# Kernel optimization log

Measured on AMD Instinct MI355X. Metric: run time of the kernel, lower is better.

Reference implementation:

```python
import jax, jax.numpy as jnp
import numpy as np
import math

B, L, HID, H, DH = 4, 1024, 1024, 16, 64
EPS = 1e-5


def setup_inputs() -> dict:
    key = jax.random.key(0)
    ks = jax.random.split(key, 12)
    s = 0.02
    return {
        "hidden_states_query": jax.random.normal(ks[0], (B, L, HID), jnp.float32),
        "hidden_states_value": jax.random.normal(ks[1], (B, L, HID), jnp.float32),
        "attention_mask": jnp.zeros((B, 1, 1, L), jnp.float32),
        "structure_matrix": jax.random.normal(ks[2], (L, L, DH), jnp.float32) * s,
        "Wq": jax.random.normal(ks[3], (H * DH, HID), jnp.float32) * s,
        "bq": jnp.zeros((H * DH,), jnp.float32),
        "Wk": jax.random.normal(ks[4], (H * DH, HID), jnp.float32) * s,
        "bk": jnp.zeros((H * DH,), jnp.float32),
        "Wv": jax.random.normal(ks[5], (H * DH, HID), jnp.float32) * s,
        "bv": jnp.zeros((H * DH,), jnp.float32),
        "Wd": jax.random.normal(ks[6], (HID, H * DH), jnp.float32) * s,
        "bd": jnp.zeros((HID,), jnp.float32),
        "ln_gamma": jnp.ones((HID,), jnp.float32),
        "ln_beta": jnp.zeros((HID,), jnp.float32),
    }


def _heads(x):
    # [B, L, H*DH] -> [B, H, L, DH]
    b, l, _ = x.shape
    return x.reshape(b, l, H, DH).transpose(0, 2, 1, 3)


def reference(hidden_states_query, hidden_states_value, attention_mask, structure_matrix,
              Wq, bq, Wk, bk, Wv, bv, Wd, bd, ln_gamma, ln_beta):
    q = _heads(hidden_states_query @ Wq.T + bq)   # [B,H,Lq,DH]
    k = _heads(hidden_states_value @ Wk.T + bk)   # [B,H,Lk,DH]
    v = _heads(hidden_states_value @ Wv.T + bv)   # [B,H,Lk,DH]

    scores = jnp.einsum('bhld,bhrd->bhlr', q, k)
    # relative-position (structure) bias terms
    scores = scores + jnp.einsum('bhld,lrd->bhlr', q, structure_matrix)
    scores = scores + jnp.einsum('bhrd,lrd->bhlr', k, structure_matrix)
    scores = scores / math.sqrt(DH)
    scores = scores + attention_mask  # broadcast [B,1,1,Lk]

    probs = jax.nn.softmax(scores, axis=-1)
    ctx = jnp.einsum('bhlr,bhrd->bhld', probs, v)
    ctx = ctx.transpose(0, 2, 1, 3).reshape(q.shape[0], q.shape[2], H * DH)

    out = ctx @ Wd.T + bd
    x = out + hidden_states_query
    mu = jnp.mean(x, axis=-1, keepdims=True)
    var = jnp.mean(jnp.square(x - mu), axis=-1, keepdims=True)
    out = (x - mu) * jax.lax.rsqrt(var + EPS) * ln_gamma + ln_beta
    return (out, scores)
```

## Files before the change

kernel.cpp:

```cpp
#include <hip/hip_runtime.h>

typedef unsigned short u16;
typedef unsigned int u32;
typedef __attribute__((ext_vector_type(8))) short bf16x8;
typedef __attribute__((ext_vector_type(4))) float f32x4;

#define DEVI static __device__ __forceinline__

DEVI u16 f2bf(float f) {
  u32 u = __float_as_uint(f);
  return (u16)((u + 0x7fffu + ((u >> 16) & 1u)) >> 16);
}
DEVI float bf2f(u16 h) { return __uint_as_float(((u32)h) << 16); }

union bfr8 { u16 u[8]; u32 w[4]; bf16x8 v; };


__global__ __launch_bounds__(256) void k_proj(
    const float* __restrict__ Xq, const float* __restrict__ Xv,
    const float* __restrict__ Wq, const float* __restrict__ bq,
    const float* __restrict__ Wk, const float* __restrict__ bk,
    const float* __restrict__ Wv, const float* __restrict__ bv,
    u16* __restrict__ Qbh, u16* __restrict__ Qlb,
    u16* __restrict__ Kbh, u16* __restrict__ Klb,
    u16* __restrict__ Vt)
{
  const int zmode = blockIdx.z;
  const float* X; const float* W; const float* bias; u16* Obh; u16* Olb;
  if (zmode == 0)      { X = Xq; W = Wq; bias = bq; Obh = Qbh; Olb = Qlb; }
  else if (zmode == 1) { X = Xv; W = Wk; bias = bk; Obh = Kbh; Olb = Klb; }
  else                 { X = Xv; W = Wv; bias = bv; Obh = Vt;  Olb = 0;   }

  __shared__ __align__(16) u16 sm[2 * 128 * 72];
  u16* As = sm;
  u16* Bs = sm + 128 * 72;
  const int t = threadIdx.x, w = t >> 6, lane = t & 63, g = lane >> 4, lr = lane & 15;
  const int n0 = blockIdx.x * 128, o0 = blockIdx.y * 128;
  const int wr = w >> 1, wc = w & 1;
  f32x4 acc[4][4] = {};
  for (int k0 = 0; k0 < 1024; k0 += 64) {
    for (int p = 0; p < 8; ++p) {
      int fi = t + p * 256, row = fi >> 4, c4 = (fi & 15) * 4;
      float4 v = *reinterpret_cast<const float4*>(X + (size_t)(n0 + row) * 1024 + k0 + c4);
      u16* d = As + row * 72 + c4;
      d[0] = f2bf(v.x); d[1] = f2bf(v.y); d[2] = f2bf(v.z); d[3] = f2bf(v.w);
    }
    for (int p = 0; p < 8; ++p) {
      int fi = t + p * 256, row = fi >> 4, c4 = (fi & 15) * 4;
      float4 v = *reinterpret_cast<const float4*>(W + (size_t)(o0 + row) * 1024 + k0 + c4);
      u16* d = Bs + row * 72 + c4;
      d[0] = f2bf(v.x); d[1] = f2bf(v.y); d[2] = f2bf(v.z); d[3] = f2bf(v.w);
    }
    __syncthreads();
    #pragma unroll
    for (int ks = 0; ks < 2; ++ks) {
      bf16x8 af[4], bfr[4];
      #pragma unroll
      for (int fm = 0; fm < 4; ++fm)
        af[fm] = *reinterpret_cast<const bf16x8*>(As + (wr * 64 + fm * 16 + lr) * 72 + ks * 32 + g * 8);
      #pragma unroll
      for (int fn = 0; fn < 4; ++fn)
        bfr[fn] = *reinterpret_cast<const bf16x8*>(Bs + (wc * 64 + fn * 16 + lr) * 72 + ks * 32 + g * 8);
      #pragma unroll
      for (int fm = 0; fm < 4; ++fm)
        #pragma unroll
        for (int fn = 0; fn < 4; ++fn)
          acc[fm][fn] = __builtin_amdgcn_mfma_f32_16x16x32_bf16(af[fm], bfr[fn], acc[fm][fn], 0, 0, 0);
    }
    __syncthreads();
  }
  float bv_[4];
  #pragma unroll
  for (int fn = 0; fn < 4; ++fn) bv_[fn] = bias[o0 + wc * 64 + fn * 16 + lr];
  u16* stg = sm + w * (64 * 72);
  if (zmode < 2) {
    #pragma unroll
    for (int fm = 0; fm < 4; ++fm)
      #pragma unroll
      for (int fn = 0; fn < 4; ++fn)
        #pragma unroll
        for (int i = 0; i < 4; ++i)
          stg[(fm * 16 + g * 4 + i) * 72 + fn * 16 + lr] = f2bf(acc[fm][fn][i] + bv_[fn]);
    __syncthreads();
    const int n = n0 + wr * 64 + lane;
    const int b = n >> 10, l = n & 1023;
    const int h = (o0 + wc * 64) >> 6;
    const int bh = b * 16 + h;
    const u16* prow = stg + lane * 72;
    u16* obh = Obh + ((size_t)bh << 16) + ((size_t)l << 6);
    u16* olb = Olb + ((size_t)l << 12) + ((size_t)bh << 6);
    #pragma unroll
    for (int c = 0; c < 8; ++c) {
      uint4 vv = *reinterpret_cast<const uint4*>(prow + c * 8);
      *reinterpret_cast<uint4*>(obh + c * 8) = vv;
      *reinterpret_cast<uint4*>(olb + c * 8) = vv;
    }
  } else {
    #pragma unroll
    for (int fm = 0; fm < 4; ++fm)
      #pragma unroll
      for (int fn = 0; fn < 4; ++fn)
        #pragma unroll
        for (int i = 0; i < 4; ++i)
          stg[(fn * 16 + lr) * 72 + fm * 16 + g * 4 + i] = f2bf(acc[fm][fn][i] + bv_[fn]);
    __syncthreads();
    const int nb = n0 + wr * 64;
    const int b = nb >> 10, l0w = nb & 1023;
    const int h = (o0 + wc * 64) >> 6;
    const int bh = b * 16 + h;
    const u16* prow = stg + lane * 72;
    u16* ovt = Obh + ((size_t)bh << 16) + ((size_t)lane << 10) + l0w;
    #pragma unroll
    for (int c = 0; c < 8; ++c)
      *reinterpret_cast<uint4*>(ovt + c * 8) = *reinterpret_cast<const uint4*>(prow + c * 8);
  }
}

__global__ __launch_bounds__(256, 3) void k_biasq(
    const float* __restrict__ S, const u16* __restrict__ Qlb,
    u16* __restrict__ bias1)
{
  __shared__ __align__(16) u16 Qs[64 * 72];
  __shared__ __align__(16) u16 stg[64 * 264];
  const int t = threadIdx.x, w = t >> 6, lane = t & 63, g = lane >> 4, lr = lane & 15;
  const int l = blockIdx.y, r0 = blockIdx.x * 256;
  {
    const u16* Qp = Qlb + (size_t)l * 4096;
    #pragma unroll
    for (int p = 0; p < 2; ++p) {
      int ci = t + p * 256, row = ci >> 3, c8 = (ci & 7) * 8;
      *reinterpret_cast<uint4*>(Qs + row * 72 + c8) =
          *reinterpret_cast<const uint4*>(Qp + row * 64 + c8);
    }
  }
  __syncthreads();
  const float* Sbase = S + ((size_t)l * 1024 + r0) * 64;
  f32x4 acc[4][4] = {};
  #pragma unroll
  for (int ks = 0; ks < 2; ++ks) {
    float4 ld[8];
    #pragma unroll
    for (int fm = 0; fm < 4; ++fm) {
      const float* p = Sbase + (size_t)(w * 64 + fm * 16 + lr) * 64 + ks * 32 + g * 8;
      ld[fm * 2 + 0] = *reinterpret_cast<const float4*>(p);
      ld[fm * 2 + 1] = *reinterpret_cast<const float4*>(p + 4);
    }
    bf16x8 af[4], bq[4];
    #pragma unroll
    for (int fm = 0; fm < 4; ++fm) {
      bfr8 u;
      u.u[0] = f2bf(ld[fm * 2].x);     u.u[1] = f2bf(ld[fm * 2].y);
      u.u[2] = f2bf(ld[fm * 2].z);     u.u[3] = f2bf(ld[fm * 2].w);
      u.u[4] = f2bf(ld[fm * 2 + 1].x); u.u[5] = f2bf(ld[fm * 2 + 1].y);
      u.u[6] = f2bf(ld[fm * 2 + 1].z); u.u[7] = f2bf(ld[fm * 2 + 1].w);
      af[fm] = u.v;
    }
    #pragma unroll
    for (int fn = 0; fn < 4; ++fn)
      bq[fn] = *reinterpret_cast<const bf16x8*>(Qs + (fn * 16 + lr) * 72 + ks * 32 + g * 8);
    #pragma unroll
    for (int fm = 0; fm < 4; ++fm)
      #pragma unroll
      for (int fn = 0; fn < 4; ++fn)
        acc[fm][fn] = __builtin_amdgcn_mfma_f32_16x16x32_bf16(af[fm], bq[fn], acc[fm][fn], 0, 0, 0);
  }
  #pragma unroll
  for (int fm = 0; fm < 4; ++fm)
    #pragma unroll
    for (int fn = 0; fn < 4; ++fn)
      #pragma unroll
      for (int i = 0; i < 4; ++i)
        stg[(fn * 16 + lr) * 264 + w * 64 + fm * 16 + g * 4 + i] = f2bf(acc[fm][fn][i] * 0.125f);
  __syncthreads();
  {
    const int bh = t >> 2, seg = t & 3;
    u16* dst = bias1 + ((size_t)bh << 21) + ((size_t)l << 11) + r0 + seg * 64;
    const u16* src = stg + bh * 264 + seg * 64;
    #pragma unroll
    for (int j = 0; j < 8; ++j)
      *reinterpret_cast<uint4*>(dst + j * 8) = *reinterpret_cast<const uint4*>(src + j * 8);
  }
}

__global__ __launch_bounds__(256, 3) void k_biask(
    const float* __restrict__ S, const u16* __restrict__ Klb,
    u16* __restrict__ TB2)
{
  __shared__ __align__(16) u16 Ksm[64 * 72];
  __shared__ __align__(16) u16 stg[64 * 264];
  const int t = threadIdx.x, w = t >> 6, lane = t & 63, g = lane >> 4, lr = lane & 15;
  const int r = blockIdx.y, l0 = blockIdx.x * 256;
  {
    const u16* Kp = Klb + (size_t)r * 4096;
    #pragma unroll
    for (int p = 0; p < 2; ++p) {
      int ci = t + p * 256, row = ci >> 3, c8 = (ci & 7) * 8;
      *reinterpret_cast<uint4*>(Ksm + row * 72 + c8) =
          *reinterpret_cast<const uint4*>(Kp + row * 64 + c8);
    }
  }
  __syncthreads();
  f32x4 acc[4][4] = {};
  #pragma unroll
  for (int ks = 0; ks < 2; ++ks) {
    float4 ld[8];
    #pragma unroll
    for (int fm = 0; fm < 4; ++fm) {
      const float* p = S + ((size_t)(l0 + w * 64 + fm * 16 + lr) << 16) + (size_t)r * 64 + ks * 32 + g * 8;
      ld[fm * 2 + 0] = *reinterpret_cast<const float4*>(p);
      ld[fm * 2 + 1] = *reinterpret_cast<const float4*>(p + 4);
    }
    bf16x8 af[4], bk[4];
    #pragma unroll
    for (int fm = 0; fm < 4; ++fm) {
      bfr8 u;
      u.u[0] = f2bf(ld[fm * 2].x);     u.u[1] = f2bf(ld[fm * 2].y);
      u.u[2] = f2bf(ld[fm * 2].z);     u.u[3] = f2bf(ld[fm * 2].w);
      u.u[4] = f2bf(ld[fm * 2 + 1].x); u.u[5] = f2bf(ld[fm * 2 + 1].y);
      u.u[6] = f2bf(ld[fm * 2 + 1].z); u.u[7] = f2bf(ld[fm * 2 + 1].w);
      af[fm] = u.v;
    }
    #pragma unroll
    for (int fn = 0; fn < 4; ++fn)
      bk[fn] = *reinterpret_cast<const bf16x8*>(Ksm + (fn * 16 + lr) * 72 + ks * 32 + g * 8);
    #pragma unroll
    for (int fm = 0; fm < 4; ++fm)
      #pragma unroll
      for (int fn = 0; fn < 4; ++fn)
        acc[fm][fn] = __builtin_amdgcn_mfma_f32_16x16x32_bf16(af[fm], bk[fn], acc[fm][fn], 0, 0, 0);
  }
  #pragma unroll
  for (int fm = 0; fm < 4; ++fm)
    #pragma unroll
    for (int fn = 0; fn < 4; ++fn)
      #pragma unroll
      for (int i = 0; i < 4; ++i)
        stg[(fn * 16 + lr) * 264 + w * 64 + fm * 16 + g * 4 + i] = f2bf(acc[fm][fn][i]);
  __syncthreads();
  {
    const int bh = t >> 2, seg = t & 3;
    u16* dst = TB2 + ((size_t)bh << 20) + ((size_t)r << 10) + l0 + seg * 64;
    const u16* src = stg + bh * 264 + seg * 64;
    #pragma unroll
    for (int j = 0; j < 8; ++j)
      *reinterpret_cast<uint4*>(dst + j * 8) = *reinterpret_cast<const uint4*>(src + j * 8);
  }
}

__global__ __launch_bounds__(256) void k_qkpv(
    const u16* __restrict__ Qbh, const u16* __restrict__ Kbh,
    const u16* __restrict__ TB2, const u16* __restrict__ Vt,
    const float* __restrict__ mask, float* __restrict__ scores,
    u16* __restrict__ ctx)
{
  __shared__ __align__(16) u16 Qs[32 * 72];
  __shared__ __align__(16) u16 Ksm[128 * 72];
  __shared__ __align__(16) u16 T2s[128 * 40];
  __shared__ __align__(16) u16 B1s[32 * 136];
  __shared__ __align__(16) u16 Vs[64 * 136];
  __shared__ float reds[32];
  __shared__ float ssum[32];
  const int t = threadIdx.x, w = t >> 6, lane = t & 63, g = lane >> 4, lr = lane & 15;
  const int bid = blockIdx.x;
  const int swz = (bid & 7) * 256 + (bid >> 3);
  const int bh = swz >> 5, l0 = (swz & 31) << 5;
  const u16* scores_u16 = reinterpret_cast<const u16*>(scores);
  {
    const u16* Qp = Qbh + ((size_t)bh << 16) + ((size_t)l0 << 6);
    int row = t >> 3, c8 = (t & 7) * 8;
    *reinterpret_cast<uint4*>(Qs + row * 72 + c8) =
        *reinterpret_cast<const uint4*>(Qp + (size_t)row * 64 + c8);
  }
  const int wr = w & 1, wc = w >> 1;
  const int l = l0 + wc * 16 + lr;
  const float* mrow = mask + ((size_t)(bh >> 4) << 10);
  float s = 0.f;
  f32x4 apv[4] = {};
  for (int r0 = 896; r0 >= 0; r0 -= 128) {
    {
      const u16* Kp = Kbh + ((size_t)bh << 16) + ((size_t)r0 << 6);
      #pragma unroll
      for (int p = 0; p < 4; ++p) {
        int ci = t + p * 256, row = ci >> 3, c8 = (ci & 7) * 8;
        *reinterpret_cast<uint4*>(Ksm + row * 72 + c8) =
            *reinterpret_cast<const uint4*>(Kp + (size_t)row * 64 + c8);
      }
    }
    {
      #pragma unroll
      for (int p = 0; p < 2; ++p) {
        int ci = t + p * 256, row = ci >> 2, c8 = (ci & 3) * 8;
        *reinterpret_cast<uint4*>(T2s + row * 40 + c8) =
            *reinterpret_cast<const uint4*>(TB2 + ((size_t)bh << 20) + ((size_t)(r0 + row) << 10) + l0 + c8);
      }
    }
    {
      #pragma unroll
      for (int p = 0; p < 2; ++p) {
        int ci = t + p * 256, row = ci >> 4, c8 = (ci & 15) * 8;
        *reinterpret_cast<uint4*>(B1s + row * 136 + c8) =
            *reinterpret_cast<const uint4*>(scores_u16 + ((size_t)bh << 21) + ((size_t)(l0 + row) << 11) + r0 + c8);
      }
    }
    {
      #pragma unroll
      for (int p = 0; p < 4; ++p) {
        int ci = t + p * 256, row = ci >> 4, c8 = (ci & 15) * 8;
        *reinterpret_cast<uint4*>(Vs + row * 136 + c8) =
            *reinterpret_cast<const uint4*>(Vt + ((size_t)bh << 16) + ((size_t)row << 10) + r0 + c8);
      }
    }
    __syncthreads();
    f32x4 acc[4] = {};
    #pragma unroll
    for (int ks = 0; ks < 2; ++ks) {
      bf16x8 bq = *reinterpret_cast<const bf16x8*>(Qs + (wc * 16 + lr) * 72 + ks * 32 + g * 8);
      #pragma unroll
      for (int fm = 0; fm < 4; ++fm) {
        bf16x8 ak = *reinterpret_cast<const bf16x8*>(Ksm + (wr * 64 + fm * 16 + lr) * 72 + ks * 32 + g * 8);
        acc[fm] = __builtin_amdgcn_mfma_f32_16x16x32_bf16(ak, bq, acc[fm], 0, 0, 0);
      }
    }
    float* srow = scores + ((size_t)bh << 20) + ((size_t)l << 10);
    u32 pL[4], pH[4];
    #pragma unroll
    for (int fm = 0; fm < 4; ++fm) {
      int rloc = wr * 64 + fm * 16 + g * 4;
      int rbase = r0 + rloc;
      float4 mv = *reinterpret_cast<const float4*>(mrow + rbase);
      float b20 = bf2f(T2s[(rloc + 0) * 40 + wc * 16 + lr]);
      float b21 = bf2f(T2s[(rloc + 1) * 40 + wc * 16 + lr]);
      float b22 = bf2f(T2s[(rloc + 2) * 40 + wc * 16 + lr]);
      float b23 = bf2f(T2s[(rloc + 3) * 40 + wc * 16 + lr]);
      uint2 b1p = *reinterpret_cast<const uint2*>(B1s + (wc * 16 + lr) * 136 + rloc);
      float b10 = bf2f((u16)(b1p.x & 0xffff)), b11 = bf2f((u16)(b1p.x >> 16));
      float b12 = bf2f((u16)(b1p.y & 0xffff)), b13 = bf2f((u16)(b1p.y >> 16));
      float4 o;
      o.x = (acc[fm][0] + b20) * 0.125f + b10 + mv.x;
      o.y = (acc[fm][1] + b21) * 0.125f + b11 + mv.y;
      o.z = (acc[fm][2] + b22) * 0.125f + b12 + mv.z;
      o.w = (acc[fm][3] + b23) * 0.125f + b13 + mv.w;
      *reinterpret_cast<float4*>(srow + rbase) = o;
      float p0 = __expf(o.x), p1 = __expf(o.y), p2 = __expf(o.z), p3 = __expf(o.w);
      s += p0 + p1 + p2 + p3;
      pL[fm] = (u32)f2bf(p0) | ((u32)f2bf(p1) << 16);
      pH[fm] = (u32)f2bf(p2) | ((u32)f2bf(p3) << 16);
    }
    #pragma unroll
    for (int t2 = 0; t2 < 2; ++t2) {
      bfr8 a;
      a.w[0] = pL[2 * t2];     a.w[1] = pH[2 * t2];
      a.w[2] = pL[2 * t2 + 1]; a.w[3] = pH[2 * t2 + 1];
      #pragma unroll
      for (int n = 0; n < 4; ++n) {
        const u16* vb = Vs + (n * 16 + lr) * 136 + wr * 64 + t2 * 32 + g * 4;
        uint2 v0 = *reinterpret_cast<const uint2*>(vb);
        uint2 v1 = *reinterpret_cast<const uint2*>(vb + 16);
        bfr8 b;
        b.w[0] = v0.x; b.w[1] = v0.y; b.w[2] = v1.x; b.w[3] = v1.y;
        apv[n] = __builtin_amdgcn_mfma_f32_16x16x32_bf16(a.v, b.v, apv[n], 0, 0, 0);
      }
    }
    __syncthreads();
  }
  #pragma unroll
  for (int off = 16; off < 64; off <<= 1) s += __shfl_xor(s, off);
  if (wr == 1 && lane < 16) reds[wc * 16 + lr] = s;
  __syncthreads();
  if (wr == 0 && lane < 16) ssum[wc * 16 + lr] = 1.0f / (s + reds[wc * 16 + lr]);
  float* c32 = reinterpret_cast<float*>(Ksm);
  u16* cb = T2s;
  if (wr == 1) {
    #pragma unroll
    for (int n = 0; n < 4; ++n)
      #pragma unroll
      for (int i = 0; i < 4; ++i)
        c32[(wc * 16 + g * 4 + i) * 66 + n * 16 + lr] = apv[n][i];
  }
  __syncthreads();
  if (wr == 0) {
    #pragma unroll
    for (int n = 0; n < 4; ++n)
      #pragma unroll
      for (int i = 0; i < 4; ++i) {
        int li = wc * 16 + g * 4 + i;
        float v = apv[n][i] + c32[li * 66 + n * 16 + lr];
        cb[li * 64 + n * 16 + lr] = f2bf(v * ssum[li]);
      }
  }
  __syncthreads();
  {
    int row = t >> 3, c8 = (t & 7) * 8;
    const int b = bh >> 4, h = bh & 15;
    uint4 vv = *reinterpret_cast<const uint4*>(cb + row * 64 + c8);
    *reinterpret_cast<uint4*>(ctx + ((size_t)(b * 1024 + l0 + row) << 10) + (h << 6) + c8) = vv;
  }
}

__global__ __launch_bounds__(256) void k_outproj(
    const u16* __restrict__ ctx, const float* __restrict__ Wd,
    const float* __restrict__ bd, const float* __restrict__ Xq,
    float* __restrict__ y)
{
  __shared__ __align__(16) u16 As_[128 * 72];
  __shared__ __align__(16) u16 Bs_[128 * 72];
  const int t = threadIdx.x, w = t >> 6, lane = t & 63, g = lane >> 4, lr = lane & 15;
  const int o0 = blockIdx.x * 128, n0 = blockIdx.y * 128;
  const int wr = w >> 1, wc = w & 1;
  f32x4 acc[4][4] = {};
  for (int k0 = 0; k0 < 1024; k0 += 64) {
    for (int p = 0; p < 8; ++p) {
      int fi = t + p * 256, row = fi >> 4, c4 = (fi & 15) * 4;
      float4 v = *reinterpret_cast<const float4*>(Wd + (size_t)(o0 + row) * 1024 + k0 + c4);
      u16* d = As_ + row * 72 + c4;
      d[0] = f2bf(v.x); d[1] = f2bf(v.y); d[2] = f2bf(v.z); d[3] = f2bf(v.w);
    }
    for (int p = 0; p < 4; ++p) {
      int ci = t + p * 256, row = ci >> 3, c8 = (ci & 7) * 8;
      *reinterpret_cast<uint4*>(Bs_ + row * 72 + c8) =
          *reinterpret_cast<const uint4*>(ctx + (size_t)(n0 + row) * 1024 + k0 + c8);
    }
    __syncthreads();
    #pragma unroll
    for (int ks = 0; ks < 2; ++ks) {
      bf16x8 af[4], bfr[4];
      #pragma unroll
      for (int fm = 0; fm < 4; ++fm)
        af[fm] = *reinterpret_cast<const bf16x8*>(As_ + (wr * 64 + fm * 16 + lr) * 72 + ks * 32 + g * 8);
      #pragma unroll
      for (int fn = 0; fn < 4; ++fn)
        bfr[fn] = *reinterpret_cast<const bf16x8*>(Bs_ + (wc * 64 + fn * 16 + lr) * 72 + ks * 32 + g * 8);
      #pragma unroll
      for (int fm = 0; fm < 4; ++fm)
        #pragma unroll
        for (int fn = 0; fn < 4; ++fn)
          acc[fm][fn] = __builtin_amdgcn_mfma_f32_16x16x32_bf16(af[fm], bfr[fn], acc[fm][fn], 0, 0, 0);
    }
    __syncthreads();
  }
  #pragma unroll
  for (int fm = 0; fm < 4; ++fm)
    #pragma unroll
    for (int fn = 0; fn < 4; ++fn) {
      int obase = o0 + wr * 64 + fm * 16 + g * 4;
      int n = n0 + wc * 64 + fn * 16 + lr;
      float4 bb = *reinterpret_cast<const float4*>(bd + obase);
      float4 xx = *reinterpret_cast<const float4*>(Xq + (size_t)n * 1024 + obase);
      float4 o;
      o.x = acc[fm][fn][0] + bb.x + xx.x;
      o.y = acc[fm][fn][1] + bb.y + xx.y;
      o.z = acc[fm][fn][2] + bb.z + xx.z;
      o.w = acc[fm][fn][3] + bb.w + xx.w;
      *reinterpret_cast<float4*>(y + (size_t)n * 1024 + obase) = o;
    }
}

__global__ __launch_bounds__(256) void k_ln(
    float* __restrict__ y, const float* __restrict__ gam,
    const float* __restrict__ bet)
{
  __shared__ float red[8];
  const int t = threadIdx.x, w = t >> 6, lane = t & 63;
  float* row = y + ((size_t)blockIdx.x << 10);
  float4 v = *reinterpret_cast<const float4*>(row + t * 4);
  float s1 = v.x + v.y + v.z + v.w;
  float s2 = v.x * v.x + v.y * v.y + v.z * v.z + v.w * v.w;
  #pragma unroll
  for (int s = 1; s < 64; s <<= 1) { s1 += __shfl_xor(s1, s); s2 += __shfl_xor(s2, s); }
  if (lane == 0) { red[w] = s1; red[4 + w] = s2; }
  __syncthreads();
  s1 = red[0] + red[1] + red[2] + red[3];
  s2 = red[4] + red[5] + red[6] + red[7];
  float mu = s1 * (1.0f / 1024.0f);
  float var = s2 * (1.0f / 1024.0f) - mu * mu;
  float rs = rsqrtf(var + 1e-5f);
  float4 gg = *reinterpret_cast<const float4*>(gam + t * 4);
  float4 bb = *reinterpret_cast<const float4*>(bet + t * 4);
  float4 o;
  o.x = (v.x - mu) * rs * gg.x + bb.x;
  o.y = (v.y - mu) * rs * gg.y + bb.y;
  o.z = (v.z - mu) * rs * gg.z + bb.z;
  o.w = (v.w - mu) * rs * gg.w + bb.w;
  *reinterpret_cast<float4*>(row + t * 4) = o;
}

extern "C" void kernel_launch(void* const* d_in, const int* in_sizes, int n_in,
                              void* d_out, int out_size, void* d_ws, size_t ws_size,
                              hipStream_t stream) {
  (void)in_sizes; (void)n_in; (void)out_size; (void)ws_size;
  const float* Xq   = (const float*)d_in[0];
  const float* Xv   = (const float*)d_in[1];
  const float* mask = (const float*)d_in[2];
  const float* S    = (const float*)d_in[3];
  const float* Wq   = (const float*)d_in[4];
  const float* bq   = (const float*)d_in[5];
  const float* Wk   = (const float*)d_in[6];
  const float* bk   = (const float*)d_in[7];
  const float* Wv   = (const float*)d_in[8];
  const float* bv   = (const float*)d_in[9];
  const float* Wd   = (const float*)d_in[10];
  const float* bd   = (const float*)d_in[11];
  const float* gam  = (const float*)d_in[12];
  const float* bet  = (const float*)d_in[13];

  float* out    = (float*)d_out;
  float* scores = out + (size_t)4 * 1024 * 1024;
  u16* scores_u16 = (u16*)scores;

  char* ws = (char*)d_ws;
  u16* Qbh = (u16*)(ws);
  u16* Kbh = (u16*)(ws + ((size_t)8 << 20));
  u16* Vt  = (u16*)(ws + ((size_t)16 << 20));
  u16* Qlb = (u16*)(ws + ((size_t)24 << 20));
  u16* Klb = (u16*)(ws + ((size_t)32 << 20));
  u16* TB2 = (u16*)(ws + ((size_t)40 << 20));
  u16* ctx = (u16*)(ws + ((size_t)169 << 20));

  k_proj<<<dim3(32, 8, 3), 256, 0, stream>>>(Xq, Xv, Wq, bq, Wk, bk, Wv, bv,
                                             Qbh, Qlb, Kbh, Klb, Vt);
  k_biasq<<<dim3(4, 1024), 256, 0, stream>>>(S, Qlb, scores_u16);
  k_biask<<<dim3(4, 1024), 256, 0, stream>>>(S, Klb, TB2);
  k_qkpv<<<2048, 256, 0, stream>>>(Qbh, Kbh, TB2, Vt, mask, scores, ctx);
  k_outproj<<<dim3(8, 32), 256, 0, stream>>>(ctx, Wd, bd, Xq, out);
  k_ln<<<4096, 256, 0, stream>>>(out, gam, bet);
}
```

Baseline: 496.2 us.

## Fuse query and key structure-bias kernels into one tiled bias-sum pass

Merges the two bias kernels into one kernel that handles a 16x16 (l,r) tile of the structure matrix. It computes both the q·S and k·S terms plus the mask and writes one summed bf16 bias tensor in transposed layout. The attention kernel then reads a single bias tile instead of two bias streams and the mask, and it iterates r forward. This removes one launch and a full bf16 bias round-trip through the scores buffer. In exchange, B operands are now read from global memory without shared-memory staging, and the structure matrix is read in two passes, one of them strided.

Result: slower. 592.5 us (+19.4%).

```diff
diff --git a/kernel.cpp b/kernel.cpp
--- a/kernel.cpp
+++ b/kernel.cpp
@@ -14,6 +14,7 @@
 DEVI float bf2f(u16 h) { return __uint_as_float(((u32)h) << 16); }
 
 union bfr8 { u16 u[8]; u32 w[4]; bf16x8 v; };
+union pk16 { u16 u[16]; uint4 q[2]; };
 
 
 __global__ __launch_bounds__(256) void k_proj(
@@ -116,147 +117,98 @@
   }
 }
 
-__global__ __launch_bounds__(256, 3) void k_biasq(
+__global__ __launch_bounds__(256) void k_bias(
     const float* __restrict__ S, const u16* __restrict__ Qlb,
-    u16* __restrict__ bias1)
+    const u16* __restrict__ Klb, const float* __restrict__ mask,
+    u16* __restrict__ TBsum)
 {
-  __shared__ __align__(16) u16 Qs[64 * 72];
-  __shared__ __align__(16) u16 stg[64 * 264];
+  __shared__ __align__(16) u16 st[16 * 16 * 72];
   const int t = threadIdx.x, w = t >> 6, lane = t & 63, g = lane >> 4, lr = lane & 15;
-  const int l = blockIdx.y, r0 = blockIdx.x * 256;
-  {
-    const u16* Qp = Qlb + (size_t)l * 4096;
-    #pragma unroll
-    for (int p = 0; p < 2; ++p) {
-      int ci = t + p * 256, row = ci >> 3, c8 = (ci & 7) * 8;
-      *reinterpret_cast<uint4*>(Qs + row * 72 + c8) =
-          *reinterpret_cast<const uint4*>(Qp + row * 64 + c8);
-    }
-  }
-  __syncthreads();
-  const float* Sbase = S + ((size_t)l * 1024 + r0) * 64;
-  f32x4 acc[4][4] = {};
-  #pragma unroll
-  for (int ks = 0; ks < 2; ++ks) {
-    float4 ld[8];
-    #pragma unroll
-    for (int fm = 0; fm < 4; ++fm) {
-      const float* p = Sbase + (size_t)(w * 64 + fm * 16 + lr) * 64 + ks * 32 + g * 8;
-      ld[fm * 2 + 0] = *reinterpret_cast<const float4*>(p);
-      ld[fm * 2 + 1] = *reinterpret_cast<const float4*>(p + 4);
-    }
-    bf16x8 af[4], bq[4];
-    #pragma unroll
-    for (int fm = 0; fm < 4; ++fm) {
-      bfr8 u;
-      u.u[0] = f2bf(ld[fm * 2].x);     u.u[1] = f2bf(ld[fm * 2].y);
-      u.u[2] = f2bf(ld[fm * 2].z);     u.u[3] = f2bf(ld[fm * 2].w);
-      u.u[4] = f2bf(ld[fm * 2 + 1].x); u.u[5] = f2bf(ld[fm * 2 + 1].y);
-      u.u[6] = f2bf(ld[fm * 2 + 1].z); u.u[7] = f2bf(ld[fm * 2 + 1].w);
-      af[fm] = u.v;
-    }
-    #pragma unroll
-    for (int fn = 0; fn < 4; ++fn)
-      bq[fn] = *reinterpret_cast<const bf16x8*>(Qs + (fn * 16 + lr) * 72 + ks * 32 + g * 8);
-    #pragma unroll
-    for (int fm = 0; fm < 4; ++fm)
-      #pragma unroll
-      for (int fn = 0; fn < 4; ++fn)
-        acc[fm][fn] = __builtin_amdgcn_mfma_f32_16x16x32_bf16(af[fm], bq[fn], acc[fm][fn], 0, 0, 0);
-  }
-  #pragma unroll
-  for (int fm = 0; fm < 4; ++fm)
-    #pragma unroll
-    for (int fn = 0; fn < 4; ++fn)
+  const int bid = blockIdx.x;
+  const int xcd = bid & 7, j = bid >> 3;
+  const int r0 = (xcd * 8 + (j >> 6)) * 16;
+  const int l0 = (j & 63) * 16;
+
+  #pragma unroll
+  for (int il = 0; il < 4; ++il) {
+    const int lloc = w * 4 + il, l = l0 + lloc;
+    f32x4 acc[4] = {};
+    #pragma unroll
+    for (int ks = 0; ks < 2; ++ks) {
+      const float* ap = S + ((size_t)l * 1024 + r0 + lr) * 64 + ks * 32 + g * 8;
+      float4 a0 = *reinterpret_cast<const float4*>(ap);
+      float4 a1 = *reinterpret_cast<const float4*>(ap + 4);
+      bfr8 a;
+      a.u[0] = f2bf(a0.x); a.u[1] = f2bf(a0.y); a.u[2] = f2bf(a0.z); a.u[3] = f2bf(a0.w);
+      a.u[4] = f2bf(a1.x); a.u[5] = f2bf(a1.y); a.u[6] = f2bf(a1.z); a.u[7] = f2bf(a1.w);
+      const u16* qb = Qlb + ((size_t)l << 12) + ks * 32 + g * 8;
+      #pragma unroll
+      for (int n = 0; n < 4; ++n) {
+        bf16x8 bq = *reinterpret_cast<const bf16x8*>(qb + (n * 16 + lr) * 64);
+        acc[n] = __builtin_amdgcn_mfma_f32_16x16x32_bf16(a.v, bq, acc[n], 0, 0, 0);
+      }
+    }
+    #pragma unroll
+    for (int n = 0; n < 4; ++n)
       #pragma unroll
       for (int i = 0; i < 4; ++i)
-        stg[(fn * 16 + lr) * 264 + w * 64 + fm * 16 + g * 4 + i] = f2bf(acc[fm][fn][i] * 0.125f);
-  __syncthreads();
-  {
-    const int bh = t >> 2, seg = t & 3;
-    u16* dst = bias1 + ((size_t)bh << 21) + ((size_t)l << 11) + r0 + seg * 64;
-    const u16* src = stg + bh * 264 + seg * 64;
-    #pragma unroll
-    for (int j = 0; j < 8; ++j)
-      *reinterpret_cast<uint4*>(dst + j * 8) = *reinterpret_cast<const uint4*>(src + j * 8);
-  }
-}
-
-__global__ __launch_bounds__(256, 3) void k_biask(
-    const float* __restrict__ S, const u16* __restrict__ Klb,
-    u16* __restrict__ TB2)
-{
-  __shared__ __align__(16) u16 Ksm[64 * 72];
-  __shared__ __align__(16) u16 stg[64 * 264];
-  const int t = threadIdx.x, w = t >> 6, lane = t & 63, g = lane >> 4, lr = lane & 15;
-  const int r = blockIdx.y, l0 = blockIdx.x * 256;
-  {
-    const u16* Kp = Klb + (size_t)r * 4096;
-    #pragma unroll
-    for (int p = 0; p < 2; ++p) {
-      int ci = t + p * 256, row = ci >> 3, c8 = (ci & 7) * 8;
-      *reinterpret_cast<uint4*>(Ksm + row * 72 + c8) =
-          *reinterpret_cast<const uint4*>(Kp + row * 64 + c8);
-    }
-  }
-  __syncthreads();
-  f32x4 acc[4][4] = {};
-  #pragma unroll
-  for (int ks = 0; ks < 2; ++ks) {
-    float4 ld[8];
-    #pragma unroll
-    for (int fm = 0; fm < 4; ++fm) {
-      const float* p = S + ((size_t)(l0 + w * 64 + fm * 16 + lr) << 16) + (size_t)r * 64 + ks * 32 + g * 8;
-      ld[fm * 2 + 0] = *reinterpret_cast<const float4*>(p);
-      ld[fm * 2 + 1] = *reinterpret_cast<const float4*>(p + 4);
-    }
-    bf16x8 af[4], bk[4];
-    #pragma unroll
-    for (int fm = 0; fm < 4; ++fm) {
-      bfr8 u;
-      u.u[0] = f2bf(ld[fm * 2].x);     u.u[1] = f2bf(ld[fm * 2].y);
-      u.u[2] = f2bf(ld[fm * 2].z);     u.u[3] = f2bf(ld[fm * 2].w);
-      u.u[4] = f2bf(ld[fm * 2 + 1].x); u.u[5] = f2bf(ld[fm * 2 + 1].y);
-      u.u[6] = f2bf(ld[fm * 2 + 1].z); u.u[7] = f2bf(ld[fm * 2 + 1].w);
-      af[fm] = u.v;
-    }
-    #pragma unroll
-    for (int fn = 0; fn < 4; ++fn)
-      bk[fn] = *reinterpret_cast<const bf16x8*>(Ksm + (fn * 16 + lr) * 72 + ks * 32 + g * 8);
-    #pragma unroll
-    for (int fm = 0; fm < 4; ++fm)
-      #pragma unroll
-      for (int fn = 0; fn < 4; ++fn)
-        acc[fm][fn] = __builtin_amdgcn_mfma_f32_16x16x32_bf16(af[fm], bk[fn], acc[fm][fn], 0, 0, 0);
-  }
-  #pragma unroll
-  for (int fm = 0; fm < 4; ++fm)
-    #pragma unroll
-    for (int fn = 0; fn < 4; ++fn)
-      #pragma unroll
-      for (int i = 0; i < 4; ++i)
-        stg[(fn * 16 + lr) * 264 + w * 64 + fm * 16 + g * 4 + i] = f2bf(acc[fm][fn][i]);
-  __syncthreads();
-  {
-    const int bh = t >> 2, seg = t & 3;
-    u16* dst = TB2 + ((size_t)bh << 20) + ((size_t)r << 10) + l0 + seg * 64;
-    const u16* src = stg + bh * 264 + seg * 64;
-    #pragma unroll
-    for (int j = 0; j < 8; ++j)
-      *reinterpret_cast<uint4*>(dst + j * 8) = *reinterpret_cast<const uint4*>(src + j * 8);
+        st[((g * 4 + i) * 16 + lloc) * 72 + n * 16 + lr] = f2bf(acc[n][i]);
+  }
+  __syncthreads();
+
+  #pragma unroll
+  for (int ir = 0; ir < 4; ++ir) {
+    const int rloc = w * 4 + ir, r = r0 + rloc;
+    f32x4 acc[4] = {};
+    #pragma unroll
+    for (int ks = 0; ks < 2; ++ks) {
+      const float* ap = S + ((size_t)(l0 + lr) * 1024 + r) * 64 + ks * 32 + g * 8;
+      float4 a0 = *reinterpret_cast<const float4*>(ap);
+      float4 a1 = *reinterpret_cast<const float4*>(ap + 4);
+      bfr8 a;
+      a.u[0] = f2bf(a0.x); a.u[1] = f2bf(a0.y); a.u[2] = f2bf(a0.z); a.u[3] = f2bf(a0.w);
+      a.u[4] = f2bf(a1.x); a.u[5] = f2bf(a1.y); a.u[6] = f2bf(a1.z); a.u[7] = f2bf(a1.w);
+      const u16* kb = Klb + ((size_t)r << 12) + ks * 32 + g * 8;
+      #pragma unroll
+      for (int n = 0; n < 4; ++n) {
+        bf16x8 bk = *reinterpret_cast<const bf16x8*>(kb + (n * 16 + lr) * 64);
+        acc[n] = __builtin_amdgcn_mfma_f32_16x16x32_bf16(a.v, bk, acc[n], 0, 0, 0);
+      }
+    }
+    #pragma unroll
+    for (int n = 0; n < 4; ++n) {
+      float mv = mask[n * 1024 + r];
+      #pragma unroll
+      for (int i = 0; i < 4; ++i) {
+        int idx = (rloc * 16 + g * 4 + i) * 72 + n * 16 + lr;
+        float qv = bf2f(st[idx]);
+        st[idx] = f2bf((acc[n][i] + qv) * 0.125f + mv);
+      }
+    }
+  }
+  __syncthreads();
+
+  #pragma unroll
+  for (int jj = 0; jj < 4; ++jj) {
+    int idx = t + jj * 256;
+    int bh = idx >> 4, rl = idx & 15;
+    pk16 tmp;
+    #pragma unroll
+    for (int l = 0; l < 16; ++l) tmp.u[l] = st[(rl * 16 + l) * 72 + bh];
+    u16* dst = TBsum + ((size_t)bh << 20) + ((size_t)(r0 + rl) << 10) + l0;
+    *reinterpret_cast<uint4*>(dst) = tmp.q[0];
+    *reinterpret_cast<uint4*>(dst + 8) = tmp.q[1];
   }
 }
 
 __global__ __launch_bounds__(256) void k_qkpv(
     const u16* __restrict__ Qbh, const u16* __restrict__ Kbh,
-    const u16* __restrict__ TB2, const u16* __restrict__ Vt,
-    const float* __restrict__ mask, float* __restrict__ scores,
-    u16* __restrict__ ctx)
+    const u16* __restrict__ TBsum, const u16* __restrict__ Vt,
+    float* __restrict__ scores, u16* __restrict__ ctx)
 {
   __shared__ __align__(16) u16 Qs[32 * 72];
   __shared__ __align__(16) u16 Ksm[128 * 72];
   __shared__ __align__(16) u16 T2s[128 * 40];
-  __shared__ __align__(16) u16 B1s[32 * 136];
   __shared__ __align__(16) u16 Vs[64 * 136];
   __shared__ float reds[32];
   __shared__ float ssum[32];
@@ -264,7 +216,6 @@
   const int bid = blockIdx.x;
   const int swz = (bid & 7) * 256 + (bid >> 3);
   const int bh = swz >> 5, l0 = (swz & 31) << 5;
-  const u16* scores_u16 = reinterpret_cast<const u16*>(scores);
   {
     const u16* Qp = Qbh + ((size_t)bh << 16) + ((size_t)l0 << 6);
     int row = t >> 3, c8 = (t & 7) * 8;
@@ -273,10 +224,9 @@
   }
   const int wr = w & 1, wc = w >> 1;
   const int l = l0 + wc * 16 + lr;
-  const float* mrow = mask + ((size_t)(bh >> 4) << 10);
   float s = 0.f;
   f32x4 apv[4] = {};
-  for (int r0 = 896; r0 >= 0; r0 -= 128) {
+  for (int r0 = 0; r0 < 1024; r0 += 128) {
     {
       const u16* Kp = Kbh + ((size_t)bh << 16) + ((size_t)r0 << 6);
       #pragma unroll
@@ -291,15 +241,7 @@
       for (int p = 0; p < 2; ++p) {
         int ci = t + p * 256, row = ci >> 2, c8 = (ci & 3) * 8;
         *reinterpret_cast<uint4*>(T2s + row * 40 + c8) =
-            *reinterpret_cast<const uint4*>(TB2 + ((size_t)bh << 20) + ((size_t)(r0 + row) << 10) + l0 + c8);
-      }
-    }
-    {
-      #pragma unroll
-      for (int p = 0; p < 2; ++p) {
-        int ci = t + p * 256, row = ci >> 4, c8 = (ci & 15) * 8;
-        *reinterpret_cast<uint4*>(B1s + row * 136 + c8) =
-            *reinterpret_cast<const uint4*>(scores_u16 + ((size_t)bh << 21) + ((size_t)(l0 + row) << 11) + r0 + c8);
+            *reinterpret_cast<const uint4*>(TBsum + ((size_t)bh << 20) + ((size_t)(r0 + row) << 10) + l0 + c8);
       }
     }
     {
@@ -327,19 +269,15 @@
     for (int fm = 0; fm < 4; ++fm) {
       int rloc = wr * 64 + fm * 16 + g * 4;
       int rbase = r0 + rloc;
-      float4 mv = *reinterpret_cast<const float4*>(mrow + rbase);
       float b20 = bf2f(T2s[(rloc + 0) * 40 + wc * 16 + lr]);
       float b21 = bf2f(T2s[(rloc + 1) * 40 + wc * 16 + lr]);
       float b22 = bf2f(T2s[(rloc + 2) * 40 + wc * 16 + lr]);
       float b23 = bf2f(T2s[(rloc + 3) * 40 + wc * 16 + lr]);
-      uint2 b1p = *reinterpret_cast<const uint2*>(B1s + (wc * 16 + lr) * 136 + rloc);
-      float b10 = bf2f((u16)(b1p.x & 0xffff)), b11 = bf2f((u16)(b1p.x >> 16));
-      float b12 = bf2f((u16)(b1p.y & 0xffff)), b13 = bf2f((u16)(b1p.y >> 16));
       float4 o;
-      o.x = (acc[fm][0] + b20) * 0.125f + b10 + mv.x;
-      o.y = (acc[fm][1] + b21) * 0.125f + b11 + mv.y;
-      o.z = (acc[fm][2] + b22) * 0.125f + b12 + mv.z;
-      o.w = (acc[fm][3] + b23) * 0.125f + b13 + mv.w;
+      o.x = acc[fm][0] * 0.125f + b20;
+      o.y = acc[fm][1] * 0.125f + b21;
+      o.z = acc[fm][2] * 0.125f + b22;
+      o.w = acc[fm][3] * 0.125f + b23;
       *reinterpret_cast<float4*>(srow + rbase) = o;
       float p0 = __expf(o.x), p1 = __expf(o.y), p2 = __expf(o.z), p3 = __expf(o.w);
       s += p0 + p1 + p2 + p3;
@@ -505,7 +443,6 @@
 
   float* out    = (float*)d_out;
   float* scores = out + (size_t)4 * 1024 * 1024;
-  u16* scores_u16 = (u16*)scores;
 
   char* ws = (char*)d_ws;
   u16* Qbh = (u16*)(ws);
@@ -513,14 +450,13 @@
   u16* Vt  = (u16*)(ws + ((size_t)16 << 20));
   u16* Qlb = (u16*)(ws + ((size_t)24 << 20));
   u16* Klb = (u16*)(ws + ((size_t)32 << 20));
-  u16* TB2 = (u16*)(ws + ((size_t)40 << 20));
+  u16* TBsum = (u16*)(ws + ((size_t)40 << 20));
   u16* ctx = (u16*)(ws + ((size_t)169 << 20));
 
   k_proj<<<dim3(32, 8, 3), 256, 0, stream>>>(Xq, Xv, Wq, bq, Wk, bk, Wv, bv,
                                              Qbh, Qlb, Kbh, Klb, Vt);
-  k_biasq<<<dim3(4, 1024), 256, 0, stream>>>(S, Qlb, scores_u16);
-  k_biask<<<dim3(4, 1024), 256, 0, stream>>>(S, Klb, TB2);
-  k_qkpv<<<2048, 256, 0, stream>>>(Qbh, Kbh, TB2, Vt, mask, scores, ctx);
+  k_bias<<<4096, 256, 0, stream>>>(S, Qlb, Klb, mask, TBsum);
+  k_qkpv<<<2048, 256, 0, stream>>>(Qbh, Kbh, TBsum, Vt, scores, ctx);
   k_outproj<<<dim3(8, 32), 256, 0, stream>>>(ctx, Wd, bd, Xq, out);
   k_ln<<<4096, 256, 0, stream>>>(out, gam, bet);
 }
```

## Stash transposed bf16 structure matrix in scratch to avoid strided fp32 reread

Applied to the files above, without the earlier changes.

The Q-bias kernel now also writes a bf16 copy of the structure matrix, laid out transposed, into spare space in the scores output buffer. The K-bias kernel then reads this compact bf16 copy instead of rereading the 256 MB fp32 tensor with a large stride. This halves the bytes of the second pass and makes its access pattern friendlier. The cost is an extra scratch write in the first kernel, and it relies on that region of the scores buffer not being overwritten before the second kernel reads it.

Result: slower. 512.4 us (+3.2%).

```diff
diff --git a/kernel.cpp b/kernel.cpp
--- a/kernel.cpp
+++ b/kernel.cpp
@@ -13,7 +13,7 @@
 }
 DEVI float bf2f(u16 h) { return __uint_as_float(((u32)h) << 16); }
 
-union bfr8 { u16 u[8]; u32 w[4]; bf16x8 v; };
+union bfr8 { u16 u[8]; u32 w[4]; uint4 q; bf16x8 v; };
 
 
 __global__ __launch_bounds__(256) void k_proj(
@@ -116,36 +116,38 @@
   }
 }
 
-__global__ __launch_bounds__(256, 3) void k_biasq(
+__global__ __launch_bounds__(256, 3) void k_bias0(
     const float* __restrict__ S, const u16* __restrict__ Qlb,
-    u16* __restrict__ bias1)
+    u16* __restrict__ scr)
 {
-  __shared__ __align__(16) u16 Qs[64 * 72];
+  __shared__ __align__(16) u16 Bsm[64 * 72];
   __shared__ __align__(16) u16 stg[64 * 264];
   const int t = threadIdx.x, w = t >> 6, lane = t & 63, g = lane >> 4, lr = lane & 15;
-  const int l = blockIdx.y, r0 = blockIdx.x * 256;
+  const int bid = blockIdx.x;
+  const int tile0 = (bid & 3) * 256;
+  const int fix = bid >> 2;
+
   {
-    const u16* Qp = Qlb + (size_t)l * 4096;
+    const u16* Bp = Qlb + (size_t)fix * 4096;
     #pragma unroll
     for (int p = 0; p < 2; ++p) {
       int ci = t + p * 256, row = ci >> 3, c8 = (ci & 7) * 8;
-      *reinterpret_cast<uint4*>(Qs + row * 72 + c8) =
-          *reinterpret_cast<const uint4*>(Qp + row * 64 + c8);
-    }
-  }
-  __syncthreads();
-  const float* Sbase = S + ((size_t)l * 1024 + r0) * 64;
+      *reinterpret_cast<uint4*>(Bsm + row * 72 + c8) =
+          *reinterpret_cast<const uint4*>(Bp + row * 64 + c8);
+    }
+  }
+  __syncthreads();
   f32x4 acc[4][4] = {};
   #pragma unroll
   for (int ks = 0; ks < 2; ++ks) {
     float4 ld[8];
     #pragma unroll
     for (int fm = 0; fm < 4; ++fm) {
-      const float* p = Sbase + (size_t)(w * 64 + fm * 16 + lr) * 64 + ks * 32 + g * 8;
+      const float* p = S + ((size_t)fix * 1024 + tile0 + w * 64 + fm * 16 + lr) * 64 + ks * 32 + g * 8;
       ld[fm * 2 + 0] = *reinterpret_cast<const float4*>(p);
       ld[fm * 2 + 1] = *reinterpret_cast<const float4*>(p + 4);
     }
-    bf16x8 af[4], bq[4];
+    bf16x8 af[4], bo[4];
     #pragma unroll
     for (int fm = 0; fm < 4; ++fm) {
       bfr8 u;
@@ -154,15 +156,19 @@
       u.u[4] = f2bf(ld[fm * 2 + 1].x); u.u[5] = f2bf(ld[fm * 2 + 1].y);
       u.u[6] = f2bf(ld[fm * 2 + 1].z); u.u[7] = f2bf(ld[fm * 2 + 1].w);
       af[fm] = u.v;
+      const int r = tile0 + w * 64 + fm * 16 + lr;
+      const size_t j = (size_t)r * 1024 + fix;
+      u16* stp = scr + (j >> 4) * 2048 + (j & 15) * 64 + 1024 + ks * 32 + g * 8;
+      *reinterpret_cast<uint4*>(stp) = u.q;
     }
     #pragma unroll
     for (int fn = 0; fn < 4; ++fn)
-      bq[fn] = *reinterpret_cast<const bf16x8*>(Qs + (fn * 16 + lr) * 72 + ks * 32 + g * 8);
+      bo[fn] = *reinterpret_cast<const bf16x8*>(Bsm + (fn * 16 + lr) * 72 + ks * 32 + g * 8);
     #pragma unroll
     for (int fm = 0; fm < 4; ++fm)
       #pragma unroll
       for (int fn = 0; fn < 4; ++fn)
-        acc[fm][fn] = __builtin_amdgcn_mfma_f32_16x16x32_bf16(af[fm], bq[fn], acc[fm][fn], 0, 0, 0);
+        acc[fm][fn] = __builtin_amdgcn_mfma_f32_16x16x32_bf16(af[fm], bo[fn], acc[fm][fn], 0, 0, 0);
   }
   #pragma unroll
   for (int fm = 0; fm < 4; ++fm)
@@ -174,7 +180,7 @@
   __syncthreads();
   {
     const int bh = t >> 2, seg = t & 3;
-    u16* dst = bias1 + ((size_t)bh << 21) + ((size_t)l << 11) + r0 + seg * 64;
+    u16* dst = scr + ((size_t)bh << 21) + ((size_t)fix << 11) + tile0 + seg * 64;
     const u16* src = stg + bh * 264 + seg * 64;
     #pragma unroll
     for (int j = 0; j < 8; ++j)
@@ -182,52 +188,46 @@
   }
 }
 
-__global__ __launch_bounds__(256, 3) void k_biask(
-    const float* __restrict__ S, const u16* __restrict__ Klb,
+__global__ __launch_bounds__(256, 3) void k_bias1(
+    const u16* __restrict__ scr, const u16* __restrict__ Klb,
     u16* __restrict__ TB2)
 {
-  __shared__ __align__(16) u16 Ksm[64 * 72];
+  __shared__ __align__(16) u16 Bsm[64 * 72];
   __shared__ __align__(16) u16 stg[64 * 264];
   const int t = threadIdx.x, w = t >> 6, lane = t & 63, g = lane >> 4, lr = lane & 15;
-  const int r = blockIdx.y, l0 = blockIdx.x * 256;
+  const int bid = blockIdx.x;
+  const int tile0 = (bid & 3) * 256;
+  const int fix = bid >> 2;
+
   {
-    const u16* Kp = Klb + (size_t)r * 4096;
+    const u16* Bp = Klb + (size_t)fix * 4096;
     #pragma unroll
     for (int p = 0; p < 2; ++p) {
       int ci = t + p * 256, row = ci >> 3, c8 = (ci & 7) * 8;
-      *reinterpret_cast<uint4*>(Ksm + row * 72 + c8) =
-          *reinterpret_cast<const uint4*>(Kp + row * 64 + c8);
+      *reinterpret_cast<uint4*>(Bsm + row * 72 + c8) =
+          *reinterpret_cast<const uint4*>(Bp + row * 64 + c8);
     }
   }
   __syncthreads();
   f32x4 acc[4][4] = {};
   #pragma unroll
   for (int ks = 0; ks < 2; ++ks) {
-    float4 ld[8];
+    bf16x8 af[4], bo[4];
     #pragma unroll
     for (int fm = 0; fm < 4; ++fm) {
-      const float* p = S + ((size_t)(l0 + w * 64 + fm * 16 + lr) << 16) + (size_t)r * 64 + ks * 32 + g * 8;
-      ld[fm * 2 + 0] = *reinterpret_cast<const float4*>(p);
-      ld[fm * 2 + 1] = *reinterpret_cast<const float4*>(p + 4);
-    }
-    bf16x8 af[4], bk[4];
-    #pragma unroll
-    for (int fm = 0; fm < 4; ++fm) {
-      bfr8 u;
-      u.u[0] = f2bf(ld[fm * 2].x);     u.u[1] = f2bf(ld[fm * 2].y);
-      u.u[2] = f2bf(ld[fm * 2].z);     u.u[3] = f2bf(ld[fm * 2].w);
-      u.u[4] = f2bf(ld[fm * 2 + 1].x); u.u[5] = f2bf(ld[fm * 2 + 1].y);
-      u.u[6] = f2bf(ld[fm * 2 + 1].z); u.u[7] = f2bf(ld[fm * 2 + 1].w);
-      af[fm] = u.v;
+      const int l = tile0 + w * 64 + fm * 16 + lr;
+      const size_t j = (size_t)fix * 1024 + l;
+      const u16* stp = scr + (j >> 4) * 2048 + (j & 15) * 64 + 1024 + ks * 32 + g * 8;
+      af[fm] = *reinterpret_cast<const bf16x8*>(stp);
     }
     #pragma unroll
     for (int fn = 0; fn < 4; ++fn)
-      bk[fn] = *reinterpret_cast<const bf16x8*>(Ksm + (fn * 16 + lr) * 72 + ks * 32 + g * 8);
+      bo[fn] = *reinterpret_cast<const bf16x8*>(Bsm + (fn * 16 + lr) * 72 + ks * 32 + g * 8);
     #pragma unroll
     for (int fm = 0; fm < 4; ++fm)
       #pragma unroll
       for (int fn = 0; fn < 4; ++fn)
-        acc[fm][fn] = __builtin_amdgcn_mfma_f32_16x16x32_bf16(af[fm], bk[fn], acc[fm][fn], 0, 0, 0);
+        acc[fm][fn] = __builtin_amdgcn_mfma_f32_16x16x32_bf16(af[fm], bo[fn], acc[fm][fn], 0, 0, 0);
   }
   #pragma unroll
   for (int fm = 0; fm < 4; ++fm)
@@ -239,7 +239,7 @@
   __syncthreads();
   {
     const int bh = t >> 2, seg = t & 3;
-    u16* dst = TB2 + ((size_t)bh << 20) + ((size_t)r << 10) + l0 + seg * 64;
+    u16* dst = TB2 + ((size_t)bh << 20) + ((size_t)fix << 10) + tile0 + seg * 64;
     const u16* src = stg + bh * 264 + seg * 64;
     #pragma unroll
     for (int j = 0; j < 8; ++j)
@@ -518,8 +518,8 @@
 
   k_proj<<<dim3(32, 8, 3), 256, 0, stream>>>(Xq, Xv, Wq, bq, Wk, bk, Wv, bv,
                                              Qbh, Qlb, Kbh, Klb, Vt);
-  k_biasq<<<dim3(4, 1024), 256, 0, stream>>>(S, Qlb, scores_u16);
-  k_biask<<<dim3(4, 1024), 256, 0, stream>>>(S, Klb, TB2);
+  k_bias0<<<4096, 256, 0, stream>>>(S, Qlb, scores_u16);
+  k_bias1<<<4096, 256, 0, stream>>>(scores_u16, Klb, TB2);
   k_qkpv<<<2048, 256, 0, stream>>>(Qbh, Kbh, TB2, Vt, mask, scores, ctx);
   k_outproj<<<dim3(8, 32), 256, 0, stream>>>(ctx, Wd, bd, Xq, out);
   k_ln<<<4096, 256, 0, stream>>>(out, gam, bet);
```
